# Kernel tuning notes

Measured on AMD Instinct MI355X. Metric: run time of the kernel, lower is better.

## Reference

```python
import jax, jax.numpy as jnp
import numpy as np


def _diag(x, ax1, ax2):
    """Extract diagonal over (ax1, ax2), placing the diag index back at ax1."""
    return jnp.moveaxis(jnp.diagonal(x, axis1=ax1, axis2=ax2), -1, ax1)


def _contractions(x):
    """All mean contractions of a 3rd-order equivariant tensor x: [B,n,n,n,C].
    Returns (a2 [B,n,n,6C], a1 [B,n,10C], a0 [B,5C])."""
    s1 = jnp.mean(x, axis=1)          # [B,n,n,C]
    s2 = jnp.mean(x, axis=2)
    s3 = jnp.mean(x, axis=3)
    d12 = _diag(x, 1, 2)              # x[b,i,i,k,c] -> [B,n,n,C]
    d13 = _diag(x, 1, 3)              # x[b,i,j,i,c]
    d23 = _diag(x, 2, 3)              # x[b,k,i,i,c]
    a2 = jnp.concatenate([s1, s2, s3, d12, d13, d23], axis=-1)  # [B,n,n,6C]

    # first-order: 3 double sums + 6 diag sums + 1 triple diag = 10C
    fo_double = [jnp.mean(x, axis=(1, 2)), jnp.mean(x, axis=(1, 3)),
                 jnp.mean(x, axis=(2, 3))]
    fo_diag = []
    for d in (d12, d13, d23):
        fo_diag.append(jnp.mean(d, axis=1))
        fo_diag.append(jnp.mean(d, axis=2))
    triple_diag = _diag(d23, 1, 2)    # x[b,i,i,i,c] -> [B,n,C]
    a1 = jnp.concatenate(fo_double + fo_diag + [triple_diag], axis=-1)  # [B,n,10C]

    # zeroth-order: triple sum + 3 diag double sums + triple-diag sum = 5C
    z = [jnp.mean(fo_double[0], axis=1)]
    z += [jnp.mean(d, axis=(1, 2)) for d in (d12, d13, d23)]
    z += [jnp.mean(triple_diag, axis=1)]
    a0 = jnp.concatenate(z, axis=-1)  # [B,5C]
    return a2, a1, a0


def _forward(x, W22, b22, W12, b12, W12t, b12t, W02, b02, W11, b11, W01, b01):
    a2, a1, a0 = _contractions(x)
    a2_w_t = jnp.concatenate([a2, jnp.swapaxes(a2, 1, 2)], axis=-1)  # [B,n,n,12C]
    # second-order mix -> [B,n,n,O]
    so = (a2_w_t @ W22 + b22
          + (a1 @ W12 + b12)[:, :, None, :]
          + (a1 @ W12t + b12t)[:, None, :, :]
          + (a0 @ W02 + b02)[:, None, None, :])
    # first-order mix -> [B,n,O], added onto the diagonal
    fo = a1 @ W11 + b11 + (a0 @ W01 + b01)[:, None, :]
    idx = jnp.arange(so.shape[1])
    return so.at[:, idx, idx, :].add(fo)


def setup_inputs() -> dict:
    key = jax.random.key(0)
    B, n, C, O = 8, 64, 32, 32
    ks = jax.random.split(key, 13)

    def w(k, fan_in):
        return (jax.random.normal(k, (fan_in, O), jnp.float32)
                / np.float32(np.sqrt(fan_in)))

    def b(k):
        return jax.random.normal(k, (O,), jnp.float32) * 0.02

    return {
        "x": jax.random.normal(ks[0], (B, n, n, n, C), jnp.float32),
        "W22": w(ks[1], 12 * C), "b22": b(ks[2]),
        "W12": w(ks[3], 10 * C), "b12": b(ks[4]),
        "W12t": w(ks[5], 10 * C), "b12t": b(ks[6]),
        "W02": w(ks[7], 5 * C), "b02": b(ks[8]),
        "W11": w(ks[9], 10 * C), "b11": b(ks[10]),
        "W01": w(ks[11], 5 * C), "b01": b(ks[12]),
    }


def reference(x, W22, b22, W12, b12, W12t, b12t, W02, b02, W11, b11, W01, b01):
    return _forward(x, W22, b22, W12, b12, W12t, b12t, W02, b02, W11, b11, W01, b01)
```

## Files before the change

kernel.cpp:

```cpp
#include <hip/hip_runtime.h>
#include <hip/hip_bf16.h>
#include <stdint.h>

#define NC   2048
#define NNC  131072
#define N3C  8388608
#define CMPE 1048576

typedef unsigned short u16;

__device__ __forceinline__ u16 bf16b(float x){
    unsigned u = __float_as_uint(x);
    u += 0x7FFFu + ((u >> 16) & 1u);
    return (u16)(u >> 16);
}
__device__ __forceinline__ float b2f(u16 h){ return __uint_as_float(((unsigned)h) << 16); }
__device__ __forceinline__ float lo16(unsigned u){ return __uint_as_float(u << 16); }
__device__ __forceinline__ float hi16(unsigned u){ return __uint_as_float(u & 0xFFFF0000u); }
__device__ __forceinline__ void f4acc(float4& a, const float4 b){
    a.x += b.x; a.y += b.y; a.z += b.z; a.w += b.w;
}
__device__ __forceinline__ void addp4(float4& a, const uint2 u){
    a.x += lo16(u.x); a.y += hi16(u.x); a.z += lo16(u.y); a.w += hi16(u.y);
}
__device__ __forceinline__ uint2 pack4(float4 v){
    uint2 r;
    r.x = (unsigned)bf16b(v.x) | ((unsigned)bf16b(v.y) << 16);
    r.y = (unsigned)bf16b(v.z) | ((unsigned)bf16b(v.w) << 16);
    return r;
}
__device__ __forceinline__ uint2 pack4s(float4 v, float s){
    v.x *= s; v.y *= s; v.z *= s; v.w *= s;
    return pack4(v);
}

__global__ __launch_bounds__(512, 2) void k_pass1(
    const float* __restrict__ x,
    u16* __restrict__ p1, u16* __restrict__ p2,
    u16* __restrict__ c_s3, u16* __restrict__ c_d12,
    u16* __restrict__ c_d13, u16* __restrict__ c_d23)
{
    int blk = blockIdx.x;
    int jg = blk & 7, ig = (blk >> 3) & 7, b = blk >> 6;
    int t = threadIdx.x;
    int kt = t >> 3, c4 = (t & 7) * 4;

    __shared__ float s3l[8][32][65];

    float4 p1a[8];
    #pragma unroll
    for (int a = 0; a < 8; ++a) p1a[a] = make_float4(0,0,0,0);

    const float* xb = x + (size_t)b * N3C + (size_t)ig * 8 * NNC + (size_t)jg * 8 * NC;

    int rjj = t >> 6, rh = (t >> 5) & 1, rc = t & 31;

    float4 v[8];
    #pragma unroll
    for (int jj = 0; jj < 8; ++jj)
        v[jj] = *reinterpret_cast<const float4*>(xb + (size_t)jj * NC + 4 * t);

    for (int ii = 0; ii < 8; ++ii){
        int i = ig * 8 + ii;
        float4 q = make_float4(0,0,0,0);
        #pragma unroll
        for (int jj = 0; jj < 8; ++jj){
            int j = jg * 8 + jj;
            f4acc(p1a[jj], v[jj]);
            f4acc(q, v[jj]);
            s3l[jj][c4 + 0][kt] = v[jj].x;
            s3l[jj][c4 + 1][kt] = v[jj].y;
            s3l[jj][c4 + 2][kt] = v[jj].z;
            s3l[jj][c4 + 3][kt] = v[jj].w;
            if (kt == i){
                *reinterpret_cast<uint2*>(c_d13 + (((size_t)(b * 64 + i)) * 64 + j) * 32 + c4) = pack4(v[jj]);
            }
            if (kt == j){
                *reinterpret_cast<uint2*>(c_d23 + (((size_t)(b * 64 + i)) * 64 + j) * 32 + c4) = pack4(v[jj]);
            }
            if (i == j){
                *reinterpret_cast<uint2*>(c_d12 + ((size_t)(b * 64 + i)) * 2048 + 4 * (size_t)t) = pack4(v[jj]);
            }
        }
        *reinterpret_cast<uint2*>(p2 + ((size_t)((b * 8 + jg) * 64 + i)) * 2048 + 4 * (size_t)t) = pack4(q);

        __syncthreads();
        float4 vn[8];
        if (ii < 7){
            #pragma unroll
            for (int jj = 0; jj < 8; ++jj)
                vn[jj] = *reinterpret_cast<const float4*>(xb + (size_t)(ii + 1) * NNC + (size_t)jj * NC + 4 * t);
        }
        {
            const float* sp = &s3l[rjj][rc][rh * 32];
            float s = 0.f;
            #pragma unroll
            for (int g = 0; g < 32; ++g) s += sp[g];
            s += __shfl_xor(s, 32, 64);
            if (rh == 0){
                c_s3[(((size_t)(b * 64 + i)) * 64 + jg * 8 + rjj) * 32 + rc] = bf16b(s * (1.f/64.f));
            }
        }
        __syncthreads();
        if (ii < 7){
            #pragma unroll
            for (int jj = 0; jj < 8; ++jj) v[jj] = vn[jj];
        }
    }
    #pragma unroll
    for (int jj = 0; jj < 8; ++jj){
        u16* o1 = p1 + ((size_t)((b * 8 + ig) * 64 + jg * 8 + jj)) * 2048;
        *reinterpret_cast<uint2*>(o1 + 4 * (size_t)t) = pack4(p1a[jj]);
    }
}

__global__ __launch_bounds__(256) void k_reduce(
    const u16* __restrict__ p1, const u16* __restrict__ p2,
    u16* __restrict__ c_s1, u16* __restrict__ c_s2)
{
    int blk = blockIdx.x;
    int b = blk >> 6, sx = (blk >> 5) & 1, ch = blk & 31;
    const u16* P = sx ? p2 : p1;
    u16* O = sx ? c_s2 : c_s1;
    int t = threadIdx.x;
    #pragma unroll
    for (int r2 = 0; r2 < 2; ++r2){
        int row = ch * 2 + r2;
        float4 a0v = make_float4(0,0,0,0), a1v = make_float4(0,0,0,0);
        #pragma unroll
        for (int g = 0; g < 8; ++g){
            const u16* src = P + ((size_t)((b * 8 + g) * 64 + row)) * 2048;
            addp4(a0v, *reinterpret_cast<const uint2*>(src + 4 * t));
            addp4(a1v, *reinterpret_cast<const uint2*>(src + 1024 + 4 * t));
        }
        u16* ob = O + ((size_t)(b * 64 + row)) * 2048;
        *reinterpret_cast<uint2*>(ob + 4 * t)        = pack4s(a0v, 1.f/64.f);
        *reinterpret_cast<uint2*>(ob + 1024 + 4 * t) = pack4s(a1v, 1.f/64.f);
    }
}

__global__ __launch_bounds__(256) void k_a1a0(
    const u16* __restrict__ comps,
    float* __restrict__ a1, float* __restrict__ a0)
{
    int b = blockIdx.x / 5, m = blockIdx.x % 5;
    const int cidx [5] = {0, 1, 3, 4, 5};
    const int rowch[5] = {1, 2, 4, 6, 8};
    const int colch[5] = {0, -1, 3, 5, 7};
    const int a0i  [5] = {0, -1, 1, 2, 3};

    const u16* M = comps + (size_t)cidx[m] * CMPE + (size_t)b * NNC;
    int t = threadIdx.x, c = t & 31, qb = (t >> 5) * 8;
    float colacc[8] = {0,0,0,0,0,0,0,0};
    __shared__ float red[2048];
    __shared__ float rowc[64][32];
    for (int p0 = 0; p0 < 64; p0 += 8){
        #pragma unroll
        for (int pp = 0; pp < 8; ++pp){
            const u16* row = M + (size_t)(p0 + pp) * 2048;
            float part = 0.f;
            #pragma unroll
            for (int kk = 0; kk < 8; ++kk){
                float v = b2f(row[(qb + kk) * 32 + c]);
                colacc[kk] += v; part += v;
            }
            red[pp * 256 + t] = part;
        }
        __syncthreads();
        {
            int pp = t >> 5, cc = t & 31;
            float ssum = 0.f;
            #pragma unroll
            for (int g = 0; g < 8; ++g) ssum += red[pp * 256 + g * 32 + cc];
            rowc[p0 + pp][cc] = ssum;
            a1[((size_t)b * 64 + p0 + pp) * 320 + rowch[m] * 32 + cc] = ssum * (1.f/64.f);
        }
        __syncthreads();
    }
    if (colch[m] >= 0){
        #pragma unroll
        for (int kk = 0; kk < 8; ++kk)
            a1[((size_t)b * 64 + qb + kk) * 320 + colch[m] * 32 + c] = colacc[kk] * (1.f/64.f);
    }
    if (a0i[m] >= 0){
        int pg = t >> 5;
        float tp = 0.f;
        #pragma unroll
        for (int r = 0; r < 8; ++r) tp += rowc[pg * 8 + r][c];
        red[t] = tp;
        __syncthreads();
        if (t < 32){
            float tot = 0.f;
            #pragma unroll
            for (int g = 0; g < 8; ++g) tot += red[g * 32 + t];
            a0[(size_t)b * 160 + a0i[m] * 32 + t] = tot * (1.f/4096.f);
        }
    }
    if (m == 2){
        __syncthreads();
        float dp = 0.f;
        #pragma unroll
        for (int r = 0; r < 8; ++r){
            int p = (t >> 5) + 8 * r;
            float dv = b2f(M[((size_t)p * 64 + p) * 32 + c]);
            a1[((size_t)b * 64 + p) * 320 + 288 + c] = dv;
            dp += dv;
        }
        red[t] = dp;
        __syncthreads();
        if (t < 32){
            float s = 0.f;
            #pragma unroll
            for (int g = 0; g < 8; ++g) s += red[g * 32 + t];
            a0[(size_t)b * 160 + 128 + t] = s * (1.f/64.f);
        }
    }
}

__global__ __launch_bounds__(256) void k_uvec(
    const float* __restrict__ a1, const float* __restrict__ a0,
    float* __restrict__ u1p, float* __restrict__ u1t, float* __restrict__ fov,
    const float* __restrict__ W12,  const float* __restrict__ b12,
    const float* __restrict__ W12t, const float* __restrict__ b12t,
    const float* __restrict__ W02,  const float* __restrict__ b02,
    const float* __restrict__ W11,  const float* __restrict__ b11,
    const float* __restrict__ W01,  const float* __restrict__ b01,
    const float* __restrict__ b22)
{
    int b = blockIdx.x >> 3, pg = blockIdx.x & 7;
    int t = threadIdx.x;
    int p = pg * 8 + (t >> 5), o = t & 31;
    const float* a1r = a1 + ((size_t)b * 64 + p) * 320;
    const float* a0r = a0 + (size_t)b * 160;
    float accP = b12[o] + b02[o] + b22[o];
    float accT = b12t[o];
    float accF = b11[o] + b01[o];
    for (int f = 0; f < 320; ++f){
        float a = a1r[f];
        accP = fmaf(a, W12 [f * 32 + o], accP);
        accT = fmaf(a, W12t[f * 32 + o], accT);
        accF = fmaf(a, W11 [f * 32 + o], accF);
    }
    for (int g = 0; g < 160; ++g){
        float a = a0r[g];
        accP = fmaf(a, W02[g * 32 + o], accP);
        accF = fmaf(a, W01[g * 32 + o], accF);
    }
    size_t idx = ((size_t)b * 64 + p) * 32 + o;
    u1p[idx] = accP; u1t[idx] = accT; fov[idx] = accF;
}

__global__ __launch_bounds__(256, 2) void k_out(
    const u16* __restrict__ comps, const float* __restrict__ W22,
    const float* __restrict__ u1p, const float* __restrict__ u1t,
    const float* __restrict__ fov, float* __restrict__ out)
{
    __shared__ __align__(16) u16 Ast[192 * 68];
    __shared__ __align__(16) u16 Bst[192 * 68];
    __shared__ __align__(16) u16 Wls[192 * 32];
    int blk = blockIdx.x;
    int b = blk >> 6, p = blk & 63;
    int t = threadIdx.x;
    int q = t >> 2, c8 = (t & 3) * 8;

    #pragma unroll
    for (int t6 = 0; t6 < 6; ++t6){
        const u16* cmp = comps + (size_t)t6 * CMPE + (size_t)b * NNC;
        uint4 av = *reinterpret_cast<const uint4*>(cmp + (size_t)p * 2048 + q * 32 + c8);
        uint4 bv = *reinterpret_cast<const uint4*>(cmp + (size_t)q * 2048 + p * 32 + c8);
        int fb = t6 * 32 + c8;
        Ast[(fb+0)*68 + q] = (u16)av.x; Ast[(fb+1)*68 + q] = (u16)(av.x >> 16);
        Ast[(fb+2)*68 + q] = (u16)av.y; Ast[(fb+3)*68 + q] = (u16)(av.y >> 16);
        Ast[(fb+4)*68 + q] = (u16)av.z; Ast[(fb+5)*68 + q] = (u16)(av.z >> 16);
        Ast[(fb+6)*68 + q] = (u16)av.w; Ast[(fb+7)*68 + q] = (u16)(av.w >> 16);
        Bst[(fb+0)*68 + q] = (u16)bv.x; Bst[(fb+1)*68 + q] = (u16)(bv.x >> 16);
        Bst[(fb+2)*68 + q] = (u16)bv.y; Bst[(fb+3)*68 + q] = (u16)(bv.y >> 16);
        Bst[(fb+4)*68 + q] = (u16)bv.z; Bst[(fb+5)*68 + q] = (u16)(bv.z >> 16);
        Bst[(fb+6)*68 + q] = (u16)bv.w; Bst[(fb+7)*68 + q] = (u16)(bv.w >> 16);
    }
    #pragma unroll
    for (int r = 0; r < 6; ++r){
        int idx = t + r * 256;
        int f = idx >> 3, o4 = (idx & 7) * 4;
        float4 w = *reinterpret_cast<const float4*>(W22 + (size_t)idx * 4);
        Wls[f*32 + o4 + 0] = bf16b(w.x); Wls[f*32 + o4 + 1] = bf16b(w.y);
        Wls[f*32 + o4 + 2] = bf16b(w.z); Wls[f*32 + o4 + 3] = bf16b(w.w);
    }
    __syncthreads();

    int qi = t & 15, oi = t >> 4;
    int q0 = qi * 4, o0 = oi * 2;
    float acc00=0,acc01=0,acc10=0,acc11=0,acc20=0,acc21=0,acc30=0,acc31=0;

    #pragma unroll 8
    for (int f = 0; f < 192; ++f){
        uint2 a4 = *reinterpret_cast<const uint2*>(Ast + f * 68 + q0);
        unsigned wp = *reinterpret_cast<const unsigned*>(Wls + f * 32 + o0);
        float w0v = lo16(wp), w1v = hi16(wp);
        float A0v = lo16(a4.x), A1v = hi16(a4.x), A2v = lo16(a4.y), A3v = hi16(a4.y);
        acc00 = fmaf(A0v, w0v, acc00); acc01 = fmaf(A0v, w1v, acc01);
        acc10 = fmaf(A1v, w0v, acc10); acc11 = fmaf(A1v, w1v, acc11);
        acc20 = fmaf(A2v, w0v, acc20); acc21 = fmaf(A2v, w1v, acc21);
        acc30 = fmaf(A3v, w0v, acc30); acc31 = fmaf(A3v, w1v, acc31);
    }
    __syncthreads();
    #pragma unroll
    for (int r = 0; r < 6; ++r){
        int idx = t + r * 256;
        int f = idx >> 3, o4 = (idx & 7) * 4;
        float4 w = *reinterpret_cast<const float4*>(W22 + 6144 + (size_t)idx * 4);
        Wls[f*32 + o4 + 0] = bf16b(w.x); Wls[f*32 + o4 + 1] = bf16b(w.y);
        Wls[f*32 + o4 + 2] = bf16b(w.z); Wls[f*32 + o4 + 3] = bf16b(w.w);
    }
    __syncthreads();
    #pragma unroll 8
    for (int f = 0; f < 192; ++f){
        uint2 a4 = *reinterpret_cast<const uint2*>(Bst + f * 68 + q0);
        unsigned wp = *reinterpret_cast<const unsigned*>(Wls + f * 32 + o0);
        float w0v = lo16(wp), w1v = hi16(wp);
        float A0v = lo16(a4.x), A1v = hi16(a4.x), A2v = lo16(a4.y), A3v = hi16(a4.y);
        acc00 = fmaf(A0v, w0v, acc00); acc01 = fmaf(A0v, w1v, acc01);
        acc10 = fmaf(A1v, w0v, acc10); acc11 = fmaf(A1v, w1v, acc11);
        acc20 = fmaf(A2v, w0v, acc20); acc21 = fmaf(A2v, w1v, acc21);
        acc30 = fmaf(A3v, w0v, acc30); acc31 = fmaf(A3v, w1v, acc31);
    }

    size_t ub = ((size_t)b * 64 + p) * 32;
    float up0 = u1p[ub + o0], up1 = u1p[ub + o0 + 1];
    const float* fovp = fov + ub;
    float accs[4][2] = {{acc00,acc01},{acc10,acc11},{acc20,acc21},{acc30,acc31}};
    #pragma unroll
    for (int iq = 0; iq < 4; ++iq){
        int qq = q0 + iq;
        size_t tb = ((size_t)b * 64 + qq) * 32;
        float e0 = up0 + u1t[tb + o0];
        float e1 = up1 + u1t[tb + o0 + 1];
        if (qq == p){ e0 += fovp[o0]; e1 += fovp[o0 + 1]; }
        float2 v; v.x = accs[iq][0] + e0; v.y = accs[iq][1] + e1;
        *reinterpret_cast<float2*>(out + (((size_t)b * 64 + p) * 64 + qq) * 32 + o0) = v;
    }
}

extern "C" void kernel_launch(void* const* d_in, const int* in_sizes, int n_in,
                              void* d_out, int out_size, void* d_ws, size_t ws_size,
                              hipStream_t stream){
    const float* x    = (const float*)d_in[0];
    const float* W22  = (const float*)d_in[1];
    const float* b22  = (const float*)d_in[2];
    const float* W12  = (const float*)d_in[3];
    const float* b12  = (const float*)d_in[4];
    const float* W12t = (const float*)d_in[5];
    const float* b12t = (const float*)d_in[6];
    const float* W02  = (const float*)d_in[7];
    const float* b02  = (const float*)d_in[8];
    const float* W11  = (const float*)d_in[9];
    const float* b11  = (const float*)d_in[10];
    const float* W01  = (const float*)d_in[11];
    const float* b01  = (const float*)d_in[12];
    float* out = (float*)d_out;
    float* ws  = (float*)d_ws;

    u16*  p1    = (u16*)ws;
    u16*  p2    = (u16*)(ws + 4194304);
    u16*  comps = (u16*)(ws + 8388608);
    float* a1   = ws + 11534336;
    float* a0   = ws + 11698176;
    float* u1p  = ws + 11699456;
    float* u1t  = ws + 11715840;
    float* fovv = ws + 11732224;

    k_pass1 <<<512, 512, 0, stream>>>(x, p1, p2,
                comps + 2*(size_t)CMPE, comps + 3*(size_t)CMPE,
                comps + 4*(size_t)CMPE, comps + 5*(size_t)CMPE);
    k_reduce<<<512, 256, 0, stream>>>(p1, p2, comps, comps + (size_t)CMPE);
    k_a1a0  <<<40,  256, 0, stream>>>(comps, a1, a0);
    k_uvec  <<<64,  256, 0, stream>>>(a1, a0, u1p, u1t, fovv,
                W12, b12, W12t, b12t, W02, b02, W11, b11, W01, b01, b22);
    k_out   <<<512, 256, 0, stream>>>(comps, W22, u1p, u1t, fovv, out);
}
```

Before: 131.1 us.

## Split pass1 over k halves, reduce s3 via wave shuffles, finish in reduce

The first pass now launches twice as many 256-thread blocks, each covering half of the k range. The k-sum for s3 is done with cross-lane shuffles and a small double-buffered shared array, which replaces the large transposed shared tile and drops one barrier per iteration. Partial s3 sums are written in fp32 to a new workspace buffer and combined in the reduce kernel, which gains a third block group for this. The explicit register prefetch of the next i-slice is removed. The aim is higher occupancy and less shared-memory traffic, at the cost of extra fp32 global writes and reads and less latency hiding within each block.

```diff
diff --git a/kernel.cpp b/kernel.cpp
--- a/kernel.cpp
+++ b/kernel.cpp
@@ -34,95 +34,97 @@
     return pack4(v);
 }
 
-__global__ __launch_bounds__(512, 2) void k_pass1(
+__global__ __launch_bounds__(256, 5) void k_pass1(
     const float* __restrict__ x,
     u16* __restrict__ p1, u16* __restrict__ p2,
-    u16* __restrict__ c_s3, u16* __restrict__ c_d12,
+    float* __restrict__ s3p, u16* __restrict__ c_d12,
     u16* __restrict__ c_d13, u16* __restrict__ c_d23)
 {
     int blk = blockIdx.x;
-    int jg = blk & 7, ig = (blk >> 3) & 7, b = blk >> 6;
+    int kh = blk & 1, jg = (blk >> 1) & 7, ig = (blk >> 4) & 7, b = blk >> 7;
     int t = threadIdx.x;
-    int kt = t >> 3, c4 = (t & 7) * 4;
-
-    __shared__ float s3l[8][32][65];
+    int lane = t & 63, w = t >> 6;
+    int kt = kh * 32 + (t >> 3), c4 = (t & 7) * 4;
+
+    __shared__ float s3l[2][4][8][32];
 
     float4 p1a[8];
     #pragma unroll
     for (int a = 0; a < 8; ++a) p1a[a] = make_float4(0,0,0,0);
 
-    const float* xb = x + (size_t)b * N3C + (size_t)ig * 8 * NNC + (size_t)jg * 8 * NC;
-
-    int rjj = t >> 6, rh = (t >> 5) & 1, rc = t & 31;
-
-    float4 v[8];
-    #pragma unroll
-    for (int jj = 0; jj < 8; ++jj)
-        v[jj] = *reinterpret_cast<const float4*>(xb + (size_t)jj * NC + 4 * t);
+    const float* xb = x + (size_t)b * N3C + (size_t)ig * 8 * NNC
+                        + (size_t)jg * 8 * NC + (size_t)kh * 1024;
+    int par = 0;
 
     for (int ii = 0; ii < 8; ++ii){
         int i = ig * 8 + ii;
+        float4 v[8];
+        #pragma unroll
+        for (int jj = 0; jj < 8; ++jj)
+            v[jj] = *reinterpret_cast<const float4*>(xb + (size_t)ii * NNC + (size_t)jj * NC + 4 * t);
         float4 q = make_float4(0,0,0,0);
         #pragma unroll
         for (int jj = 0; jj < 8; ++jj){
             int j = jg * 8 + jj;
             f4acc(p1a[jj], v[jj]);
             f4acc(q, v[jj]);
-            s3l[jj][c4 + 0][kt] = v[jj].x;
-            s3l[jj][c4 + 1][kt] = v[jj].y;
-            s3l[jj][c4 + 2][kt] = v[jj].z;
-            s3l[jj][c4 + 3][kt] = v[jj].w;
-            if (kt == i){
+            float4 r = v[jj];
+            r.x += __shfl_xor(r.x, 8, 64);  r.y += __shfl_xor(r.y, 8, 64);
+            r.z += __shfl_xor(r.z, 8, 64);  r.w += __shfl_xor(r.w, 8, 64);
+            r.x += __shfl_xor(r.x, 16, 64); r.y += __shfl_xor(r.y, 16, 64);
+            r.z += __shfl_xor(r.z, 16, 64); r.w += __shfl_xor(r.w, 16, 64);
+            r.x += __shfl_xor(r.x, 32, 64); r.y += __shfl_xor(r.y, 32, 64);
+            r.z += __shfl_xor(r.z, 32, 64); r.w += __shfl_xor(r.w, 32, 64);
+            if ((lane >> 3) == 0)
+                *reinterpret_cast<float4*>(&s3l[par][w][jj][(lane & 7) * 4]) = r;
+            if (kt == i)
                 *reinterpret_cast<uint2*>(c_d13 + (((size_t)(b * 64 + i)) * 64 + j) * 32 + c4) = pack4(v[jj]);
-            }
-            if (kt == j){
+            if (kt == j)
                 *reinterpret_cast<uint2*>(c_d23 + (((size_t)(b * 64 + i)) * 64 + j) * 32 + c4) = pack4(v[jj]);
-            }
-            if (i == j){
-                *reinterpret_cast<uint2*>(c_d12 + ((size_t)(b * 64 + i)) * 2048 + 4 * (size_t)t) = pack4(v[jj]);
-            }
-        }
-        *reinterpret_cast<uint2*>(p2 + ((size_t)((b * 8 + jg) * 64 + i)) * 2048 + 4 * (size_t)t) = pack4(q);
-
-        __syncthreads();
-        float4 vn[8];
-        if (ii < 7){
-            #pragma unroll
-            for (int jj = 0; jj < 8; ++jj)
-                vn[jj] = *reinterpret_cast<const float4*>(xb + (size_t)(ii + 1) * NNC + (size_t)jj * NC + 4 * t);
-        }
+            if (i == j)
+                *reinterpret_cast<uint2*>(c_d12 + ((size_t)(b * 64 + i)) * 2048 + kh * 1024 + 4 * (size_t)t) = pack4(v[jj]);
+        }
+        *reinterpret_cast<uint2*>(p2 + ((size_t)((b * 8 + jg) * 64 + i)) * 2048 + kh * 1024 + 4 * (size_t)t) = pack4(q);
+
+        __syncthreads();
         {
-            const float* sp = &s3l[rjj][rc][rh * 32];
-            float s = 0.f;
-            #pragma unroll
-            for (int g = 0; g < 32; ++g) s += sp[g];
-            s += __shfl_xor(s, 32, 64);
-            if (rh == 0){
-                c_s3[(((size_t)(b * 64 + i)) * 64 + jg * 8 + rjj) * 32 + rc] = bf16b(s * (1.f/64.f));
-            }
-        }
-        __syncthreads();
-        if (ii < 7){
-            #pragma unroll
-            for (int jj = 0; jj < 8; ++jj) v[jj] = vn[jj];
-        }
-    }
-    #pragma unroll
-    for (int jj = 0; jj < 8; ++jj){
-        u16* o1 = p1 + ((size_t)((b * 8 + ig) * 64 + jg * 8 + jj)) * 2048;
-        *reinterpret_cast<uint2*>(o1 + 4 * (size_t)t) = pack4(p1a[jj]);
-    }
+            int jj = t >> 5, c = t & 31;
+            float s = s3l[par][0][jj][c] + s3l[par][1][jj][c]
+                    + s3l[par][2][jj][c] + s3l[par][3][jj][c];
+            s3p[(size_t)kh * 1048576 + ((size_t)(b * 64 + i)) * 2048 + (jg * 8 + jj) * 32 + c] = s;
+        }
+        par ^= 1;
+    }
+    #pragma unroll
+    for (int jj = 0; jj < 8; ++jj)
+        *reinterpret_cast<uint2*>(p1 + ((size_t)((b * 8 + ig) * 64 + jg * 8 + jj)) * 2048 + kh * 1024 + 4 * (size_t)t) = pack4(p1a[jj]);
 }
 
 __global__ __launch_bounds__(256) void k_reduce(
     const u16* __restrict__ p1, const u16* __restrict__ p2,
-    u16* __restrict__ c_s1, u16* __restrict__ c_s2)
+    const float* __restrict__ s3p,
+    u16* __restrict__ c_s1, u16* __restrict__ c_s2, u16* __restrict__ c_s3)
 {
     int blk = blockIdx.x;
-    int b = blk >> 6, sx = (blk >> 5) & 1, ch = blk & 31;
+    int b = blk / 96, rr = blk % 96, sx = rr >> 5, ch = rr & 31;
+    int t = threadIdx.x;
+    if (sx == 2){
+        #pragma unroll
+        for (int r2 = 0; r2 < 2; ++r2){
+            int row = ch * 2 + r2;
+            #pragma unroll
+            for (int e = 0; e < 2; ++e){
+                size_t base = ((size_t)(b * 64 + row)) * 2048 + e * 1024 + 4 * t;
+                float4 a = *reinterpret_cast<const float4*>(s3p + base);
+                float4 c2 = *reinterpret_cast<const float4*>(s3p + 1048576 + base);
+                f4acc(a, c2);
+                *reinterpret_cast<uint2*>(c_s3 + base) = pack4s(a, 1.f/64.f);
+            }
+        }
+        return;
+    }
     const u16* P = sx ? p2 : p1;
     u16* O = sx ? c_s2 : c_s1;
-    int t = threadIdx.x;
     #pragma unroll
     for (int r2 = 0; r2 < 2; ++r2){
         int row = ch * 2 + r2;
@@ -363,16 +365,17 @@
     u16*  p1    = (u16*)ws;
     u16*  p2    = (u16*)(ws + 4194304);
     u16*  comps = (u16*)(ws + 8388608);
-    float* a1   = ws + 11534336;
-    float* a0   = ws + 11698176;
-    float* u1p  = ws + 11699456;
-    float* u1t  = ws + 11715840;
-    float* fovv = ws + 11732224;
-
-    k_pass1 <<<512, 512, 0, stream>>>(x, p1, p2,
-                comps + 2*(size_t)CMPE, comps + 3*(size_t)CMPE,
-                comps + 4*(size_t)CMPE, comps + 5*(size_t)CMPE);
-    k_reduce<<<512, 256, 0, stream>>>(p1, p2, comps, comps + (size_t)CMPE);
+    float* s3p  = ws + 11534336;
+    float* a1   = ws + 13631488;
+    float* a0   = ws + 13795328;
+    float* u1p  = ws + 13796608;
+    float* u1t  = ws + 13812992;
+    float* fovv = ws + 13829376;
+
+    k_pass1 <<<1024, 256, 0, stream>>>(x, p1, p2, s3p,
+                comps + 3*(size_t)CMPE, comps + 4*(size_t)CMPE, comps + 5*(size_t)CMPE);
+    k_reduce<<<768, 256, 0, stream>>>(p1, p2, s3p,
+                comps, comps + (size_t)CMPE, comps + 2*(size_t)CMPE);
     k_a1a0  <<<40,  256, 0, stream>>>(comps, a1, a0);
     k_uvec  <<<64,  256, 0, stream>>>(a1, a0, u1p, u1t, fovv,
                 W12, b12, W12t, b12t, W02, b02, W11, b11, W01, b01, b22);
```

Result: slower. 140.7 us (+7.3%).
